# Kernel tuning notes

Hardware: AMD Instinct MI355X
Metric: run time of the kernel (lower is better)

Reference implementation:

```python
import jax, jax.numpy as jnp
import numpy as np

EPS = 1e-5  # torch BatchNorm2d default eps


def adder2d(x, w, stride=1, padding=1):
    """AdderNet conv: out[n,co,h,w] = -sum_k |patch(x) - w[co]| (no multiplies).

    x: [N, Cin, H, W], w: [Cout, Cin, kh, kw] -> [N, Cout, Ho, Wo]
    """
    cout, _, kh, kw = w.shape
    # patches: [N, Cin*kh*kw, Ho, Wo], feature dim ordered (Cin, kh, kw)
    patches = jax.lax.conv_general_dilated_patches(
        x, (kh, kw), (stride, stride),
        ((padding, padding), (padding, padding)))
    wf = w.reshape(cout, -1)  # [Cout, Cin*kh*kw] (same ordering as patches)

    # Loop over output channels to avoid a [N,Cout,Ckk,Ho,Wo] intermediate.
    @jax.checkpoint
    def per_out(wc):  # wc: [Cin*kh*kw]
        return -jnp.sum(jnp.abs(patches - wc[None, :, None, None]), axis=1)

    out = jax.lax.map(per_out, wf)  # [Cout, N, Ho, Wo]
    return jnp.transpose(out, (1, 0, 2, 3))


def bn_inference(x, gamma, beta, mean, var):
    inv = gamma * jax.lax.rsqrt(var + EPS)
    return x * inv[None, :, None, None] + (beta - mean * inv)[None, :, None, None]


def setup_inputs() -> dict:
    key = jax.random.key(0)
    ks = jax.random.split(key, 16)
    N, C, H, W = 16, 128, 32, 32
    R = C // 16  # SE bottleneck
    return {
        "x": jax.random.normal(ks[0], (N, C, H, W), jnp.float32),
        "w1": jax.random.normal(ks[1], (C, C, 3, 3), jnp.float32) * 0.05,
        "bn1_gamma": jax.random.uniform(ks[2], (C,), jnp.float32),
        "bn1_beta": jax.random.normal(ks[3], (C,), jnp.float32) * 0.1,
        "bn1_mean": jax.random.normal(ks[4], (C,), jnp.float32) * 0.1,
        "bn1_var": jax.random.uniform(ks[5], (C,), jnp.float32),
        "w2": jax.random.normal(ks[6], (C, C, 3, 3), jnp.float32) * 0.05,
        "bn2_gamma": jax.random.uniform(ks[7], (C,), jnp.float32),
        "bn2_beta": jax.random.normal(ks[8], (C,), jnp.float32) * 0.1,
        "bn2_mean": jax.random.normal(ks[9], (C,), jnp.float32) * 0.1,
        "bn2_var": jax.random.uniform(ks[10], (C,), jnp.float32),
        "fc1_w": jax.random.normal(ks[11], (R, C), jnp.float32) * 0.1,
        "fc1_b": jax.random.normal(ks[12], (R,), jnp.float32) * 0.1,
        "fc2_w": jax.random.normal(ks[13], (C, R), jnp.float32) * 0.1,
        "fc2_b": jax.random.normal(ks[14], (C,), jnp.float32) * 0.1,
    }


def reference(x, w1, bn1_gamma, bn1_beta, bn1_mean, bn1_var,
              w2, bn2_gamma, bn2_beta, bn2_mean, bn2_var,
              fc1_w, fc1_b, fc2_w, fc2_b):
    out = jax.nn.relu(bn_inference(adder2d(x, w1), bn1_gamma, bn1_beta, bn1_mean, bn1_var))
    out = bn_inference(adder2d(out, w2), bn2_gamma, bn2_beta, bn2_mean, bn2_var)
    # SE gate: global avg pool -> fc1 -> relu -> fc2 -> sigmoid
    s = jnp.mean(out, axis=(2, 3))                       # [N, C]
    s = jax.nn.relu(s @ fc1_w.T + fc1_b)                 # [N, C//16]
    s = jax.nn.sigmoid(s @ fc2_w.T + fc2_b)              # [N, C]
    out = out * s[:, :, None, None]
    # identity shortcut (stride=1, in_planes == planes)
    return jax.nn.relu(out + x)
```

## Files before the change

kernel.cpp:

```cpp
#include <hip/hip_runtime.h>
#include <math.h>

#define BN_EPS 1e-5f

typedef float v2f __attribute__((ext_vector_type(2)));

__global__ void wtrans2_kernel(const float* __restrict__ w1, float* __restrict__ wt1,
                               const float* __restrict__ w2, float* __restrict__ wt2) {
    int gi = blockIdx.x * 256 + threadIdx.x;
    const int N = 128 * 128 * 9;
    if (gi >= 2 * N) return;
    const float* w = (gi < N) ? w1 : w2;
    float* wt = (gi < N) ? wt1 : wt2;
    int i = (gi < N) ? gi : gi - N;
    int co = i / 1152;
    int rem = i - co * 1152;
    int ci = rem / 9;
    int k = rem - ci * 9;
    float v = w[i];
    int q = ci >> 1, z = ci & 1;
    if (k < 8) {
        int kk = k >> 1, h = k & 1;
        wt[q * 2048 + kk * 512 + co * 4 + h * 2 + z] = v;
    } else {
        wt[131072 + q * 256 + co * 2 + z] = v;
    }
}

__global__ void prep_kernel(const float* __restrict__ x, float* __restrict__ xpi,
                            float* __restrict__ yp) {
    const int plane = blockIdx.x;
    const int n = plane >> 6, q = plane & 63;
    const float* sp0 = x + ((size_t)n * 128 + 2 * q) * 1024;
    const float* sp1 = sp0 + 1024;
    float* dp = xpi + (size_t)plane * 2448;
    for (int e = threadIdx.x; e < 2448; e += 256) {
        const int idx = e >> 1, z = e & 1;
        const int pr = idx / 36, pc = idx - pr * 36;
        const int r = pr - 1, c = pc - 1;
        float v = 0.f;
        if ((unsigned)r < 32u && (unsigned)c < 32u) v = (z ? sp1 : sp0)[r * 32 + c];
        dp[e] = v;
    }
    float* bp = yp + (size_t)plane * 2448;
    const int t = threadIdx.x;
    if (t < 72) { bp[t] = 0.f; bp[33 * 72 + t] = 0.f; }
    else if (t < 136) {
        int r = 1 + ((t - 72) >> 1), z = (t - 72) & 1;
        bp[r * 72 + z] = 0.f;
    } else if (t < 200) {
        int r = 1 + ((t - 136) >> 1), z = (t - 136) & 1;
        bp[r * 72 + 66 + z] = 0.f;
    }
}

__device__ __forceinline__ void load_rowI(v2f (&R)[10], const float* rp) {
    *(float4*)&R[0] = *(const float4*)(rp);
    *(float4*)&R[2] = *(const float4*)(rp + 4);
    *(float4*)&R[4] = *(const float4*)(rp + 8);
    *(float4*)&R[6] = *(const float4*)(rp + 12);
    *(float4*)&R[8] = *(const float4*)(rp + 16);
}

__device__ __forceinline__ void rowacc(float (&acc)[8], const v2f (&R)[10],
                                       v2f w0, v2f w1, v2f w2) {
#pragma unroll
    for (int j = 0; j < 8; ++j) {
        v2f d0 = R[j] - w0;
        v2f d1 = R[j + 1] - w1;
        v2f d2 = R[j + 2] - w2;
        acc[j] += fabsf(d0.x); acc[j] += fabsf(d0.y);
        acc[j] += fabsf(d1.x); acc[j] += fabsf(d1.y);
        acc[j] += fabsf(d2.x); acc[j] += fabsf(d2.y);
    }
}

__global__ __launch_bounds__(256, 2) void adder_conv_part(
    const float* __restrict__ src,
    const float* __restrict__ wt,
    float* __restrict__ dst0, float* __restrict__ dst1) {
    const int t = threadIdx.x;
    const int lane = t & 63;
    const int wq = t >> 6;

    const int bid = blockIdx.x;
    const int xcd = bid & 7;
    const int slot = bid >> 3;
    const int nbit = slot >> 7;
    const int rem = slot & 127;
    const int half = rem >> 6;
    const int cohalf = (rem >> 5) & 1;
    const int row = rem & 31;
    const int n = xcd * 2 + nbit;

    const int co = (cohalf << 6) + lane;
    const int qb = half * 32;

    const float* sbase = src + ((size_t)n * 64 + qb) * 2448;
    const float* wb  = wt + (size_t)qb * 2048 + co * 4;
    const float* wb8 = wt + 131072 + (size_t)qb * 256 + co * 2;

    const int offA = row * 72 + wq * 16;
    const int offB = offA + 72;
    const int offC = offB + 72;

    float acc[8];
#pragma unroll
    for (int j = 0; j < 8; ++j) acc[j] = 0.f;

    v2f A2[10], B2[10], C2[10], wk[9];

    load_rowI(A2, sbase + offA);
    load_rowI(B2, sbase + offB);
    load_rowI(C2, sbase + offC);
    {
        const float4 g0 = *(const float4*)(wb);
        const float4 g1 = *(const float4*)(wb + 512);
        const float4 g2 = *(const float4*)(wb + 1024);
        const float4 g3 = *(const float4*)(wb + 1536);
        const float2 g4 = *(const float2*)(wb8);
        wk[0] = (v2f){g0.x, g0.y}; wk[1] = (v2f){g0.z, g0.w};
        wk[2] = (v2f){g1.x, g1.y}; wk[3] = (v2f){g1.z, g1.w};
        wk[4] = (v2f){g2.x, g2.y}; wk[5] = (v2f){g2.z, g2.w};
        wk[6] = (v2f){g3.x, g3.y}; wk[7] = (v2f){g3.z, g3.w};
        wk[8] = (v2f){g4.x, g4.y};
    }

#pragma unroll 1
    for (int p = 0; p < 32; ++p) {
        const int pn = (p + 1 < 32) ? p + 1 : 31;
        const float* spn = sbase + (size_t)pn * 2448;
        const float* wpn = wb + (size_t)pn * 2048;
        const float* wpn8 = wb8 + (size_t)pn * 256;

        rowacc(acc, A2, wk[0], wk[1], wk[2]);
        load_rowI(A2, spn + offA);
        const float4 g0 = *(const float4*)(wpn);
        const float4 g1 = *(const float4*)(wpn + 512);
        rowacc(acc, B2, wk[3], wk[4], wk[5]);
        load_rowI(B2, spn + offB);
        const float4 g2 = *(const float4*)(wpn + 1024);
        const float4 g3 = *(const float4*)(wpn + 1536);
        const float2 g4 = *(const float2*)(wpn8);
        rowacc(acc, C2, wk[6], wk[7], wk[8]);
        load_rowI(C2, spn + offC);
        wk[0] = (v2f){g0.x, g0.y}; wk[1] = (v2f){g0.z, g0.w};
        wk[2] = (v2f){g1.x, g1.y}; wk[3] = (v2f){g1.z, g1.w};
        wk[4] = (v2f){g2.x, g2.y}; wk[5] = (v2f){g2.z, g2.w};
        wk[6] = (v2f){g3.x, g3.y}; wk[7] = (v2f){g3.z, g3.w};
        wk[8] = (v2f){g4.x, g4.y};
    }

    const int c0 = wq << 3;
    float* dst = half ? dst1 : dst0;
    float* dp = dst + (((size_t)n * 32 + row) * 32 + c0) * 128 + co;
#pragma unroll
    for (int j = 0; j < 8; ++j) dp[j * 128] = acc[j];
}

template <bool RELU, bool PADDED>
__global__ void combine_bn_t(const float* __restrict__ pA, const float* __restrict__ pB,
                             const float* __restrict__ gamma, const float* __restrict__ beta,
                             const float* __restrict__ mean, const float* __restrict__ var,
                             float* __restrict__ out, float* __restrict__ rs) {
    const int t = threadIdx.x;
    const int row = blockIdx.x;
    const int n = blockIdx.y;
    __shared__ float tile[32 * 129];
    const size_t base = (((size_t)n * 32 + row) * 32) * 128;

    const int co = t & 127, th = t >> 7;
    const float iv = gamma[co] * rsqrtf(var[co] + BN_EPS);
    const float bb = beta[co] - mean[co] * iv;
    float psum = 0.f;
#pragma unroll
    for (int e = 0; e < 16; ++e) {
        const int px = e * 2 + th;
        const size_t idx = base + px * 128 + co;
        float z = bb - (pA[idx] + pB[idx]) * iv;
        if (RELU) z = fmaxf(z, 0.f);
        if (!PADDED) psum += z;
        tile[px * 129 + co] = z;
    }
    if (!PADDED) rs[((size_t)(n * 32 + row) * 2 + th) * 128 + co] = psum;
    __syncthreads();
#pragma unroll
    for (int e = 0; e < 4; ++e) {
        const int qidx = e * 256 + t;
        const int oco = qidx >> 3, q = qidx & 7;
        float4 v;
        v.x = tile[(4 * q + 0) * 129 + oco];
        v.y = tile[(4 * q + 1) * 129 + oco];
        v.z = tile[(4 * q + 2) * 129 + oco];
        v.w = tile[(4 * q + 3) * 129 + oco];
        if (PADDED) {
            float* op = &out[((((size_t)n * 64 + (oco >> 1)) * 34 + row + 1) * 36
                              + 1 + 4 * q) * 2 + (oco & 1)];
            op[0] = v.x; op[2] = v.y; op[4] = v.z; op[6] = v.w;
        } else {
            *(float4*)&out[(((size_t)n * 128 + oco) * 32 + row) * 32 + 4 * q] = v;
        }
    }
}

__global__ void se_kernel(const float* __restrict__ rs,
                          const float* __restrict__ fc1w, const float* __restrict__ fc1b,
                          const float* __restrict__ fc2w, const float* __restrict__ fc2b,
                          float* __restrict__ s) {
    const int n = blockIdx.x;
    const int t = threadIdx.x;
    __shared__ float m[128], rr[8];
    float a0 = 0.f;
    for (int j = 0; j < 64; ++j) a0 += rs[((size_t)n * 64 + j) * 128 + t];
    m[t] = a0 * (1.f / 1024.f);
    __syncthreads();
    if (t < 8) {
        float a = fc1b[t];
        for (int c2 = 0; c2 < 128; ++c2) a += fc1w[t * 128 + c2] * m[c2];
        rr[t] = fmaxf(a, 0.f);
    }
    __syncthreads();
    float a = fc2b[t];
#pragma unroll
    for (int j = 0; j < 8; ++j) a += fc2w[t * 8 + j] * rr[j];
    s[n * 128 + t] = 1.f / (1.f + expf(-a));
}

__global__ void final_kernel(const float* __restrict__ z, const float* __restrict__ x,
                             const float* __restrict__ s, float* __restrict__ out) {
    const int i = blockIdx.x * 256 + threadIdx.x;
    const int plane = i >> 8;
    const float sc = s[plane];
    const float4 zv = ((const float4*)z)[i];
    const float4 xv = ((const float4*)x)[i];
    float4 o;
    o.x = fmaxf(zv.x * sc + xv.x, 0.f);
    o.y = fmaxf(zv.y * sc + xv.y, 0.f);
    o.z = fmaxf(zv.z * sc + xv.z, 0.f);
    o.w = fmaxf(zv.w * sc + xv.w, 0.f);
    ((float4*)out)[i] = o;
}

extern "C" void kernel_launch(void* const* d_in, const int* in_sizes, int n_in,
                              void* d_out, int out_size, void* d_ws, size_t ws_size,
                              hipStream_t stream) {
    const float* x    = (const float*)d_in[0];
    const float* w1   = (const float*)d_in[1];
    const float* g1   = (const float*)d_in[2];
    const float* b1   = (const float*)d_in[3];
    const float* m1   = (const float*)d_in[4];
    const float* v1   = (const float*)d_in[5];
    const float* w2   = (const float*)d_in[6];
    const float* g2   = (const float*)d_in[7];
    const float* b2   = (const float*)d_in[8];
    const float* m2   = (const float*)d_in[9];
    const float* v2   = (const float*)d_in[10];
    const float* fc1w = (const float*)d_in[11];
    const float* fc1b = (const float*)d_in[12];
    const float* fc2w = (const float*)d_in[13];
    const float* fc2b = (const float*)d_in[14];
    float* out = (float*)d_out;

    float* ws    = (float*)d_ws;
    float* wt1   = ws;
    float* wt2   = wt1 + 147456;
    float* xpi   = wt2 + 147456;
    float* yp    = xpi + 2506752;
    float* pA    = yp + 2506752;
    float* pB    = pA + 2097152;
    float* rs    = pB + 2097152;
    float* s     = rs + 131072;
    float* z     = xpi;

    wtrans2_kernel<<<1152, 256, 0, stream>>>(w1, wt1, w2, wt2);
    prep_kernel<<<1024, 256, 0, stream>>>(x, xpi, yp);

    dim3 tgrid(32, 16);
    adder_conv_part<<<2048, 256, 0, stream>>>(xpi, wt1, pA, pB);
    combine_bn_t<true, true ><<<tgrid, 256, 0, stream>>>(pA, pB, g1, b1, m1, v1, yp, rs);
    adder_conv_part<<<2048, 256, 0, stream>>>(yp, wt2, pA, pB);
    combine_bn_t<false, false><<<tgrid, 256, 0, stream>>>(pA, pB, g2, b2, m2, v2, z, rs);

    se_kernel<<<16, 128, 0, stream>>>(rs, fc1w, fc1b, fc2w, fc2b, s);
    final_kernel<<<2048, 256, 0, stream>>>(z, x, s, out);
}
```

Measured before the change: 342.5 us.

## Stage adder-conv weights into LDS via async global_load_lds double buffering

Weights used to be loaded per wave straight from global memory into registers each channel-pair iteration. Now the four waves of a block share the job of staging two channel-pairs of weights at a time into a double-buffered LDS slab with global_load_lds, then read them back from LDS. The loop now covers two pairs per iteration with one block barrier. This removes redundant global weight loads across waves and the register pressure of prefetching weights, at the cost of LDS usage and a __syncthreads each iteration.

```diff
diff --git a/kernel.cpp b/kernel.cpp
--- a/kernel.cpp
+++ b/kernel.cpp
@@ -75,6 +75,17 @@
     }
 }
 
+__device__ __forceinline__ void gl_lds16(const float* g, float* l) {
+    __builtin_amdgcn_global_load_lds(
+        (const __attribute__((address_space(1))) void*)g,
+        (__attribute__((address_space(3))) void*)l, 16, 0, 0);
+}
+__device__ __forceinline__ void gl_lds4(const float* g, float* l) {
+    __builtin_amdgcn_global_load_lds(
+        (const __attribute__((address_space(1))) void*)g,
+        (__attribute__((address_space(3))) void*)l, 4, 0, 0);
+}
+
 __global__ __launch_bounds__(256, 2) void adder_conv_part(
     const float* __restrict__ src,
     const float* __restrict__ wt,
@@ -97,58 +108,82 @@
     const int qb = half * 32;
 
     const float* sbase = src + ((size_t)n * 64 + qb) * 2448;
-    const float* wb  = wt + (size_t)qb * 2048 + co * 4;
-    const float* wb8 = wt + 131072 + (size_t)qb * 256 + co * 2;
 
     const int offA = row * 72 + wq * 16;
     const int offB = offA + 72;
     const int offC = offB + 72;
 
+    __shared__ __align__(16) float wl[2][2][1152];
+
+    auto stage = [&](int buf, int p0) {
+#pragma unroll
+        for (int k = 0; k < 3; ++k) {
+            const int i = wq * 3 + k;
+            const int pp = i / 6, c = i % 6;
+            if (c < 4) {
+                const float* s = wt + (size_t)(qb + p0 + pp) * 2048 + c * 512
+                                 + cohalf * 256 + lane * 4;
+                gl_lds16(s, &wl[buf][pp][c * 256]);
+            } else {
+                const int h = c - 4;
+                const float* s = wt + 131072 + (size_t)(qb + p0 + pp) * 256
+                                 + cohalf * 128 + h * 64 + lane;
+                gl_lds4(s, &wl[buf][pp][1024 + h * 64]);
+            }
+        }
+    };
+
     float acc[8];
 #pragma unroll
     for (int j = 0; j < 8; ++j) acc[j] = 0.f;
 
-    v2f A2[10], B2[10], C2[10], wk[9];
-
+    v2f A2[10], B2[10], C2[10];
+
+    stage(0, 0);
     load_rowI(A2, sbase + offA);
     load_rowI(B2, sbase + offB);
     load_rowI(C2, sbase + offC);
-    {
-        const float4 g0 = *(const float4*)(wb);
-        const float4 g1 = *(const float4*)(wb + 512);
-        const float4 g2 = *(const float4*)(wb + 1024);
-        const float4 g3 = *(const float4*)(wb + 1536);
-        const float2 g4 = *(const float2*)(wb8);
-        wk[0] = (v2f){g0.x, g0.y}; wk[1] = (v2f){g0.z, g0.w};
-        wk[2] = (v2f){g1.x, g1.y}; wk[3] = (v2f){g1.z, g1.w};
-        wk[4] = (v2f){g2.x, g2.y}; wk[5] = (v2f){g2.z, g2.w};
-        wk[6] = (v2f){g3.x, g3.y}; wk[7] = (v2f){g3.z, g3.w};
-        wk[8] = (v2f){g4.x, g4.y};
-    }
+    __syncthreads();
 
 #pragma unroll 1
-    for (int p = 0; p < 32; ++p) {
-        const int pn = (p + 1 < 32) ? p + 1 : 31;
-        const float* spn = sbase + (size_t)pn * 2448;
-        const float* wpn = wb + (size_t)pn * 2048;
-        const float* wpn8 = wb8 + (size_t)pn * 256;
-
-        rowacc(acc, A2, wk[0], wk[1], wk[2]);
-        load_rowI(A2, spn + offA);
-        const float4 g0 = *(const float4*)(wpn);
-        const float4 g1 = *(const float4*)(wpn + 512);
-        rowacc(acc, B2, wk[3], wk[4], wk[5]);
-        load_rowI(B2, spn + offB);
-        const float4 g2 = *(const float4*)(wpn + 1024);
-        const float4 g3 = *(const float4*)(wpn + 1536);
-        const float2 g4 = *(const float2*)(wpn8);
-        rowacc(acc, C2, wk[6], wk[7], wk[8]);
-        load_rowI(C2, spn + offC);
-        wk[0] = (v2f){g0.x, g0.y}; wk[1] = (v2f){g0.z, g0.w};
-        wk[2] = (v2f){g1.x, g1.y}; wk[3] = (v2f){g1.z, g1.w};
-        wk[4] = (v2f){g2.x, g2.y}; wk[5] = (v2f){g2.z, g2.w};
-        wk[6] = (v2f){g3.x, g3.y}; wk[7] = (v2f){g3.z, g3.w};
-        wk[8] = (v2f){g4.x, g4.y};
+    for (int g = 0; g < 16; ++g) {
+        const bool more = (g < 15);
+        if (more) stage((g + 1) & 1, 2 * (g + 1));
+
+        const float* slab0 = &wl[g & 1][0][0];
+        const float* slab1 = &wl[g & 1][1][0];
+
+        {
+            const float4 e0 = *(const float4*)&slab0[lane * 4];
+            const float4 e1 = *(const float4*)&slab0[256 + lane * 4];
+            const float4 e2 = *(const float4*)&slab0[512 + lane * 4];
+            const float4 e3 = *(const float4*)&slab0[768 + lane * 4];
+            const float2 e4 = *(const float2*)&slab0[1024 + lane * 2];
+            const int pr = 2 * g + 1;
+            const float* spn = sbase + (size_t)pr * 2448;
+            rowacc(acc, A2, (v2f){e0.x, e0.y}, (v2f){e0.z, e0.w}, (v2f){e1.x, e1.y});
+            load_rowI(A2, spn + offA);
+            rowacc(acc, B2, (v2f){e1.z, e1.w}, (v2f){e2.x, e2.y}, (v2f){e2.z, e2.w});
+            load_rowI(B2, spn + offB);
+            rowacc(acc, C2, (v2f){e3.x, e3.y}, (v2f){e3.z, e3.w}, (v2f){e4.x, e4.y});
+            load_rowI(C2, spn + offC);
+        }
+        {
+            const float4 o0 = *(const float4*)&slab1[lane * 4];
+            const float4 o1 = *(const float4*)&slab1[256 + lane * 4];
+            const float4 o2 = *(const float4*)&slab1[512 + lane * 4];
+            const float4 o3 = *(const float4*)&slab1[768 + lane * 4];
+            const float2 o4 = *(const float2*)&slab1[1024 + lane * 2];
+            const int pr = (2 * g + 2 < 32) ? 2 * g + 2 : 31;
+            const float* spn = sbase + (size_t)pr * 2448;
+            rowacc(acc, A2, (v2f){o0.x, o0.y}, (v2f){o0.z, o0.w}, (v2f){o1.x, o1.y});
+            load_rowI(A2, spn + offA);
+            rowacc(acc, B2, (v2f){o1.z, o1.w}, (v2f){o2.x, o2.y}, (v2f){o2.z, o2.w});
+            load_rowI(B2, spn + offB);
+            rowacc(acc, C2, (v2f){o3.x, o3.y}, (v2f){o3.z, o3.w}, (v2f){o4.x, o4.y});
+            load_rowI(C2, spn + offC);
+        }
+        __syncthreads();
     }
 
     const int c0 = wq << 3;
```

After: 395.0 us. 15.3% more time.
